# Kernel optimization log

Hardware: AMD Instinct MI355X
Metric: run time of the kernel (lower is better)

Reference implementation:

```python
import jax, jax.numpy as jnp
import numpy as np

B, M, N, E, H, HID = 4, 512, 512, 256, 16, 16
D = E // H


def setup_inputs() -> dict:
    key = jax.random.key(0)
    ks = jax.random.split(key, 10)
    u = lambda k, shape, lim: jax.random.uniform(k, shape, jnp.float32, -lim, lim)
    mix1_init = (1.0 / 2.0) ** 0.5
    mix2_init = (1.0 / 16.0) ** 0.5
    return {
        "q_input": jax.random.normal(ks[0], (B, M, E), jnp.float32),
        "kv_input": jax.random.normal(ks[1], (B, N, E), jnp.float32),
        "dmat": jax.random.uniform(ks[2], (B, M, N), jnp.float32),
        "Wq": u(ks[3], (E, E), 1.0 / np.sqrt(E)),
        "Wkv": u(ks[4], (2 * E, E), 1.0 / np.sqrt(E)),
        "mix_W1": u(ks[5], (H, 2, HID), mix1_init),
        "mix_b1": u(ks[6], (H, HID), mix1_init),
        "mix_W2": u(ks[7], (H, HID, 1), mix2_init),
        "mix_b2": u(ks[8], (H, 1), mix2_init),
        "Wout": u(ks[9], (E, E), 1.0 / np.sqrt(E)),
    }


def reference(q_input, kv_input, dmat, Wq, Wkv, mix_W1, mix_b1, mix_W2, mix_b2, Wout):
    b, m, e = q_input.shape
    n = kv_input.shape[1]
    h = mix_W1.shape[0]
    d = e // h
    # projections (torch Linear: y = x @ W.T)
    q = (q_input @ Wq.T).reshape(b, m, h, d).transpose(0, 2, 1, 3)        # b h m d
    kv = (kv_input @ Wkv.T).reshape(b, n, 2, h, d)                        # (two h d) split
    k = kv[:, :, 0].transpose(0, 2, 1, 3)                                 # b h n d
    v = kv[:, :, 1].transpose(0, 2, 1, 3)                                 # b h n d
    scale = jnp.sqrt(jnp.asarray(d, q.dtype))
    scores = jnp.einsum('bhmd,bhnd->bhmn', q, k) / scale                  # b h m n
    # mix scores with dmat via per-head 2-layer MLP on the last (size-2) axis
    mix = jnp.stack([scores, jnp.broadcast_to(dmat[:, None], scores.shape)], axis=-1)  # b h m n 2
    hidden = jax.nn.relu(jnp.einsum('bhmnt,htk->bhmnk', mix, mix_W1)
                         + mix_b1[None, :, None, None, :])                # b h m n HID
    mixed = (jnp.einsum('bhmnk,hko->bhmno', hidden, mix_W2)
             + mix_b2[None, :, None, None, :])[..., 0]                    # b h m n
    probs = jax.nn.softmax(mixed, axis=-1)
    out = jnp.einsum('bhmn,bhnd->bhmd', probs, v)                         # b h m d
    out = out.transpose(0, 2, 1, 3).reshape(b, m, e)                      # b m (h d)
    return out @ Wout.T
```

## Files before the change

kernel.cpp:

```cpp
#include <hip/hip_runtime.h>
#include <stdint.h>
#include <stddef.h>

#define MM 512
#define NN 512
#define EE 256
#define HH 16
#define DD 16

typedef __bf16 bf16x8 __attribute__((ext_vector_type(8)));
typedef float f32x4 __attribute__((ext_vector_type(4)));

static __device__ __forceinline__ bf16x8 bzero8() {
  bf16x8 z;
#pragma unroll
  for (int i = 0; i < 8; ++i) z[i] = (__bf16)0.0f;
  return z;
}

static __device__ __forceinline__ bf16x8 cvt8(const float* __restrict__ p) {
  const float4 u = *(const float4*)p;
  const float4 v = *(const float4*)(p + 4);
  bf16x8 r;
  r[0] = (__bf16)u.x; r[1] = (__bf16)u.y; r[2] = (__bf16)u.z; r[3] = (__bf16)u.w;
  r[4] = (__bf16)v.x; r[5] = (__bf16)v.y; r[6] = (__bf16)v.z; r[7] = (__bf16)v.w;
  return r;
}

static __device__ __forceinline__ unsigned short f2b(float f) {
  union { __bf16 h; unsigned short u; } cv;
  cv.h = (__bf16)f;
  return cv.u;
}

static __device__ __forceinline__ float b2f(unsigned short u) {
  union { unsigned int i; float f; } cv;
  cv.i = ((unsigned int)u) << 16;
  return cv.f;
}

static __device__ __forceinline__ float fexp2(float x) {
  float r;
  asm("v_exp_f32 %0, %1" : "=v"(r) : "v"(x));
  return r;
}

static __device__ __forceinline__ unsigned int cvtpk(float lo, float hi) {
  unsigned int r;
  asm("v_cvt_pk_bf16_f32 %0, %1, %2" : "=v"(r) : "v"(lo), "v"(hi));
  return r;
}

static __device__ __forceinline__ float sload(const float* p) {
  return __int_as_float(__builtin_amdgcn_readfirstlane(__float_as_int(*p)));
}

__global__ __launch_bounds__(256) void proj_all_kernel(
    const float* __restrict__ Xq, const float* __restrict__ Xkv,
    const float* __restrict__ Wq, const float* __restrict__ Wkv,
    const float* __restrict__ Wout,
    unsigned short* __restrict__ Qs, unsigned short* __restrict__ Ks,
    unsigned short* __restrict__ Vt,
    unsigned short* __restrict__ Whi, unsigned short* __restrict__ Wlo) {
  const int by = blockIdx.y;
  const int tid = threadIdx.x;

  if (by == 12) {
    const int base = (blockIdx.x * 256 + tid) * 4;
    const float4 v = *(const float4*)(Wout + base);
    float c4[4] = {v.x, v.y, v.z, v.w};
#pragma unroll
    for (int i = 0; i < 4; ++i) {
      const unsigned short hb = f2b(c4[i]);
      Whi[base + i] = hb;
      Wlo[base + i] = f2b(c4[i] - b2f(hb));
    }
    return;
  }

  const int w = tid >> 6, l = tid & 63;
  const int lg = l >> 4, lr = l & 15;
  const int t0 = blockIdx.x * 32 + (w & 1) * 16;

  if (by < 4) {
    const int n0 = by * 64 + (w >> 1) * 32;
    f32x4 acc0 = {0.f, 0.f, 0.f, 0.f}, acc1 = {0.f, 0.f, 0.f, 0.f};
#pragma unroll
    for (int kc = 0; kc < EE; kc += 32) {
      const int k = kc + lg * 8;
      bf16x8 a  = cvt8(Xq + (size_t)(t0 + lr) * EE + k);
      bf16x8 b0 = cvt8(Wq + (size_t)(n0 + lr) * EE + k);
      bf16x8 b1 = cvt8(Wq + (size_t)(n0 + 16 + lr) * EE + k);
      acc0 = __builtin_amdgcn_mfma_f32_16x16x32_bf16(a, b0, acc0, 0, 0, 0);
      acc1 = __builtin_amdgcn_mfma_f32_16x16x32_bf16(a, b1, acc1, 0, 0, 0);
    }
#pragma unroll
    for (int r = 0; r < 4; ++r) {
      const int t = t0 + 4 * lg + r, b = t >> 9, m = t & 511;
      const int j0 = n0 + lr, j1 = j0 + 16;
      Qs[((size_t)(b * HH + (j0 >> 4)) * MM + m) * DD + (j0 & 15)] = f2b(acc0[r] * 0.25f);
      Qs[((size_t)(b * HH + (j1 >> 4)) * MM + m) * DD + (j1 & 15)] = f2b(acc1[r] * 0.25f);
    }
  } else {
    const int n0 = (by - 4) * 64 + (w >> 1) * 32;
    f32x4 acc0 = {0.f, 0.f, 0.f, 0.f}, acc1 = {0.f, 0.f, 0.f, 0.f};
#pragma unroll
    for (int kc = 0; kc < EE; kc += 32) {
      const int k = kc + lg * 8;
      bf16x8 a  = cvt8(Xkv + (size_t)(t0 + lr) * EE + k);
      bf16x8 b0 = cvt8(Wkv + (size_t)(n0 + lr) * EE + k);
      bf16x8 b1 = cvt8(Wkv + (size_t)(n0 + 16 + lr) * EE + k);
      acc0 = __builtin_amdgcn_mfma_f32_16x16x32_bf16(a, b0, acc0, 0, 0, 0);
      acc1 = __builtin_amdgcn_mfma_f32_16x16x32_bf16(a, b1, acc1, 0, 0, 0);
    }
#pragma unroll
    for (int r = 0; r < 4; ++r) {
      const int t = t0 + 4 * lg + r, b = t >> 9, n = t & 511;
#pragma unroll
      for (int fi = 0; fi < 2; ++fi) {
        const int j = n0 + lr + fi * 16;
        const float v = fi ? acc1[r] : acc0[r];
        if (j < 256) {
          Ks[((size_t)(b * HH + (j >> 4)) * NN + n) * DD + (j & 15)] = f2b(v);
        } else {
          const int jj = j - 256;
          Vt[((size_t)(b * HH + (jj >> 4)) * DD + (jj & 15)) * NN + n] = f2b(v);
        }
      }
    }
  }
}

__global__ __launch_bounds__(256, 2) void attn_kernel(
    const unsigned short* __restrict__ Qs, const unsigned short* __restrict__ Ks,
    const unsigned short* __restrict__ Vt, const float* __restrict__ dmat,
    const float* __restrict__ W1, const float* __restrict__ b1v,
    const float* __restrict__ W2,
    unsigned short* __restrict__ Ahi, unsigned short* __restrict__ Alo) {
  __shared__ unsigned short P[32][520];
  __shared__ float red[4][32];
  float (*pvred)[2][16][16] = (float (*)[2][16][16]) & P[0][0];

  const int tid = threadIdx.x, w = tid >> 6, l = tid & 63;
  const int lg = l >> 4, lr = l & 15;
  const int bid = blockIdx.x;
  const int mt = bid & 15, hh = (bid >> 4) & 15, b = bid >> 8;
  const int m0 = mt * 32;
  const int n0 = w * 128;

  const unsigned short* Qbase = Qs + ((size_t)(b * HH + hh) * MM + m0) * DD;
  const unsigned short* Kbase = Ks + (size_t)(b * HH + hh) * NN * DD;
  const unsigned short* Vbase = Vt + (size_t)(b * HH + hh) * DD * NN;
  const float* dbase = dmat + (size_t)b * MM * NN;

  float ckv[16], bkv[16], wkp[16];
  float Ac = 0.f, Cc = 0.f;
  const float hiln2 = 0.5f * 1.4426950408889634f;
#pragma unroll
  for (int k = 0; k < 16; ++k) {
    const float ak = sload(W1 + hh * 32 + k);
    const float ck = sload(W1 + hh * 32 + 16 + k);
    const float bk = sload(b1v + hh * 16 + k);
    const float wk = hiln2 * sload(W2 + hh * 16 + k);
    Ac += wk * ak;
    Cc += wk * ck;
    const float ra = 1.0f / ak;
    ckv[k] = ck * ra;
    bkv[k] = bk * ra;
    wkp[k] = wk * fabsf(ak);
    asm volatile("" : "+v"(ckv[k]));
    asm volatile("" : "+v"(bkv[k]));
  }

  bf16x8 qb[2];
#pragma unroll
  for (int mb = 0; mb < 2; ++mb) {
    qb[mb] = bzero8();
    if (lg < 2) qb[mb] = *(const bf16x8*)(Qbase + (mb * 16 + lr) * DD + lg * 8);
  }

  const f32x4 zf = {0.f, 0.f, 0.f, 0.f};
  float psum[2] = {0.f, 0.f};

#pragma unroll
  for (int nb = 0; nb < 8; ++nb) {
    bf16x8 ka = bzero8();
    if (lg < 2)
      ka = *(const bf16x8*)(Kbase + (size_t)(n0 + nb * 16 + lr) * DD + lg * 8);
    f32x4 cc[2];
    cc[0] = __builtin_amdgcn_mfma_f32_16x16x32_bf16(ka, qb[0], zf, 0, 0, 0);
    cc[1] = __builtin_amdgcn_mfma_f32_16x16x32_bf16(ka, qb[1], zf, 0, 0, 0);
#pragma unroll
    for (int mb = 0; mb < 2; ++mb) {
      const int mrow = m0 + mb * 16 + lr;
      const int ncol = n0 + nb * 16 + 4 * lg;
      const float4 dv = *(const float4*)(dbase + (size_t)mrow * NN + ncol);
      float ev[4];
#pragma unroll
      for (int r = 0; r < 4; ++r) {
        const float s = cc[mb][r];
        const float d = (r == 0) ? dv.x : (r == 1) ? dv.y : (r == 2) ? dv.z : dv.w;
        float acc = fmaf(Ac, s, Cc * d);
#pragma unroll
        for (int k = 0; k < 16; ++k) {
          const float t = fmaf(ckv[k], d, bkv[k]);
          acc = fmaf(wkp[k], fabsf(s + t), acc);
        }
        const float e = fexp2(acc);
        psum[mb] += e;
        ev[r] = e;
      }
      uint2 u;
      u.x = cvtpk(ev[0], ev[1]);
      u.y = cvtpk(ev[2], ev[3]);
      *(uint2*)&P[mb * 16 + lr][n0 + nb * 16 + 4 * lg] = u;
    }
  }

#pragma unroll
  for (int mb = 0; mb < 2; ++mb) {
    psum[mb] += __shfl_xor(psum[mb], 16);
    psum[mb] += __shfl_xor(psum[mb], 32);
    if (lg == 0) red[w][mb * 16 + lr] = psum[mb];
  }

  f32x4 pv[2];
  pv[0] = zf; pv[1] = zf;
#pragma unroll
  for (int kb = 0; kb < 4; ++kb) {
    const bf16x8 vb = *(const bf16x8*)(Vbase + (size_t)lr * NN + (n0 + kb * 32 + lg * 8));
#pragma unroll
    for (int mb = 0; mb < 2; ++mb) {
      const bf16x8 pa = *(const bf16x8*)(&P[mb * 16 + lr][n0 + kb * 32 + lg * 8]);
      pv[mb] = __builtin_amdgcn_mfma_f32_16x16x32_bf16(pa, vb, pv[mb], 0, 0, 0);
    }
  }
  __syncthreads();
#pragma unroll
  for (int mb = 0; mb < 2; ++mb)
#pragma unroll
    for (int r = 0; r < 4; ++r) pvred[w][mb][4 * lg + r][lr] = pv[mb][r];
  __syncthreads();

  for (int i = tid; i < 512; i += 256) {
    const int mr = i >> 4, dd = i & 15;
    const float s = pvred[0][mr >> 4][mr & 15][dd] + pvred[1][mr >> 4][mr & 15][dd] +
                    pvred[2][mr >> 4][mr & 15][dd] + pvred[3][mr >> 4][mr & 15][dd];
    const float rs = red[0][mr] + red[1][mr] + red[2][mr] + red[3][mr];
    const float val = s / rs;
    const unsigned short hb = f2b(val);
    const size_t o = ((size_t)(b * MM) + m0 + mr) * EE + hh * DD + dd;
    Ahi[o] = hb;
    Alo[o] = f2b(val - b2f(hb));
  }
}

__global__ __launch_bounds__(256) void out_gemm_kernel(
    const unsigned short* __restrict__ Ahi, const unsigned short* __restrict__ Alo,
    const unsigned short* __restrict__ Whi, const unsigned short* __restrict__ Wlo,
    float* __restrict__ out) {
  const int tid = threadIdx.x, w = tid >> 6, l = tid & 63;
  const int lg = l >> 4, lr = l & 15;
  const int t0 = blockIdx.x * 32 + (w & 1) * 16;
  const int n0 = blockIdx.y * 64 + (w >> 1) * 32;
  f32x4 acc0 = {0.f, 0.f, 0.f, 0.f}, acc1 = {0.f, 0.f, 0.f, 0.f};
#pragma unroll
  for (int kc = 0; kc < EE; kc += 32) {
    const int k = kc + lg * 8;
    const bf16x8 ah = *(const bf16x8*)(Ahi + (size_t)(t0 + lr) * EE + k);
    const bf16x8 al = *(const bf16x8*)(Alo + (size_t)(t0 + lr) * EE + k);
    const bf16x8 bh0 = *(const bf16x8*)(Whi + (size_t)(n0 + lr) * EE + k);
    const bf16x8 bh1 = *(const bf16x8*)(Whi + (size_t)(n0 + 16 + lr) * EE + k);
    const bf16x8 bl0 = *(const bf16x8*)(Wlo + (size_t)(n0 + lr) * EE + k);
    const bf16x8 bl1 = *(const bf16x8*)(Wlo + (size_t)(n0 + 16 + lr) * EE + k);
    acc0 = __builtin_amdgcn_mfma_f32_16x16x32_bf16(ah, bh0, acc0, 0, 0, 0);
    acc0 = __builtin_amdgcn_mfma_f32_16x16x32_bf16(al, bh0, acc0, 0, 0, 0);
    acc0 = __builtin_amdgcn_mfma_f32_16x16x32_bf16(ah, bl0, acc0, 0, 0, 0);
    acc1 = __builtin_amdgcn_mfma_f32_16x16x32_bf16(ah, bh1, acc1, 0, 0, 0);
    acc1 = __builtin_amdgcn_mfma_f32_16x16x32_bf16(al, bh1, acc1, 0, 0, 0);
    acc1 = __builtin_amdgcn_mfma_f32_16x16x32_bf16(ah, bl1, acc1, 0, 0, 0);
  }
#pragma unroll
  for (int r = 0; r < 4; ++r) {
    const int row = t0 + 4 * lg + r;
    out[(size_t)row * EE + n0 + lr] = acc0[r];
    out[(size_t)row * EE + n0 + 16 + lr] = acc1[r];
  }
}

extern "C" void kernel_launch(void* const* d_in, const int* in_sizes, int n_in,
                              void* d_out, int out_size, void* d_ws, size_t ws_size,
                              hipStream_t stream) {
  const float* q_input  = (const float*)d_in[0];
  const float* kv_input = (const float*)d_in[1];
  const float* dmat     = (const float*)d_in[2];
  const float* Wq       = (const float*)d_in[3];
  const float* Wkv      = (const float*)d_in[4];
  const float* W1       = (const float*)d_in[5];
  const float* b1       = (const float*)d_in[6];
  const float* W2       = (const float*)d_in[7];
  const float* Wout     = (const float*)d_in[9];
  float* out = (float*)d_out;

  char* ws = (char*)d_ws;
  unsigned short* Qs  = (unsigned short*)(ws);
  unsigned short* Ks  = (unsigned short*)(ws + (1u << 20));
  unsigned short* Vt  = (unsigned short*)(ws + (2u << 20));
  unsigned short* Ahi = (unsigned short*)(ws + (3u << 20));
  unsigned short* Alo = (unsigned short*)(ws + (4u << 20));
  unsigned short* Whi = (unsigned short*)(ws + (5u << 20));
  unsigned short* Wlo = (unsigned short*)(ws + (5u << 20) + (1u << 17));

  proj_all_kernel<<<dim3(64, 13), 256, 0, stream>>>(q_input, kv_input, Wq, Wkv, Wout,
                                                    Qs, Ks, Vt, Whi, Wlo);
  attn_kernel<<<dim3(1024), 256, 0, stream>>>(Qs, Ks, Vt, dmat, W1, b1, W2,
                                              Ahi, Alo);
  out_gemm_kernel<<<dim3(64, 4), 256, 0, stream>>>(Ahi, Alo, Whi, Wlo, out);
}
```

Baseline: 63.35 us.

## Fuse Q projection and output GEMM into attention kernel with last-block counter

Computes the Q projection inside the attention kernel (stored in LDS), so each 512-thread block handles 4 heads for a 32-row tile and reuses the dmat tile loaded once into registers. The output projection is done by whichever block finishes last for each (batch, m-tile), found through an atomic counter, which removes a separate kernel launch. The KV projection kernel also zeroes the counters. In exchange the grid shrinks to 256 blocks, each block runs its heads one after another, and the final GEMM runs on only 64 blocks at the tail.

```diff
diff --git a/kernel.cpp b/kernel.cpp
--- a/kernel.cpp
+++ b/kernel.cpp
@@ -55,17 +55,17 @@
   return __int_as_float(__builtin_amdgcn_readfirstlane(__float_as_int(*p)));
 }
 
-__global__ __launch_bounds__(256) void proj_all_kernel(
-    const float* __restrict__ Xq, const float* __restrict__ Xkv,
-    const float* __restrict__ Wq, const float* __restrict__ Wkv,
+__global__ __launch_bounds__(256) void proj_kv_kernel(
+    const float* __restrict__ Xkv, const float* __restrict__ Wkv,
     const float* __restrict__ Wout,
-    unsigned short* __restrict__ Qs, unsigned short* __restrict__ Ks,
-    unsigned short* __restrict__ Vt,
-    unsigned short* __restrict__ Whi, unsigned short* __restrict__ Wlo) {
+    unsigned short* __restrict__ Ks, unsigned short* __restrict__ Vt,
+    unsigned short* __restrict__ Whi, unsigned short* __restrict__ Wlo,
+    unsigned int* __restrict__ cnt) {
   const int by = blockIdx.y;
   const int tid = threadIdx.x;
 
-  if (by == 12) {
+  if (by == 8) {
+    if (blockIdx.x == 0 && tid < 64) cnt[tid] = 0u;
     const int base = (blockIdx.x * 256 + tid) * 4;
     const float4 v = *(const float4*)(Wout + base);
     float c4[4] = {v.x, v.y, v.z, v.w};
@@ -81,210 +81,222 @@
   const int w = tid >> 6, l = tid & 63;
   const int lg = l >> 4, lr = l & 15;
   const int t0 = blockIdx.x * 32 + (w & 1) * 16;
-
-  if (by < 4) {
-    const int n0 = by * 64 + (w >> 1) * 32;
-    f32x4 acc0 = {0.f, 0.f, 0.f, 0.f}, acc1 = {0.f, 0.f, 0.f, 0.f};
-#pragma unroll
-    for (int kc = 0; kc < EE; kc += 32) {
-      const int k = kc + lg * 8;
-      bf16x8 a  = cvt8(Xq + (size_t)(t0 + lr) * EE + k);
-      bf16x8 b0 = cvt8(Wq + (size_t)(n0 + lr) * EE + k);
-      bf16x8 b1 = cvt8(Wq + (size_t)(n0 + 16 + lr) * EE + k);
-      acc0 = __builtin_amdgcn_mfma_f32_16x16x32_bf16(a, b0, acc0, 0, 0, 0);
-      acc1 = __builtin_amdgcn_mfma_f32_16x16x32_bf16(a, b1, acc1, 0, 0, 0);
-    }
-#pragma unroll
-    for (int r = 0; r < 4; ++r) {
-      const int t = t0 + 4 * lg + r, b = t >> 9, m = t & 511;
-      const int j0 = n0 + lr, j1 = j0 + 16;
-      Qs[((size_t)(b * HH + (j0 >> 4)) * MM + m) * DD + (j0 & 15)] = f2b(acc0[r] * 0.25f);
-      Qs[((size_t)(b * HH + (j1 >> 4)) * MM + m) * DD + (j1 & 15)] = f2b(acc1[r] * 0.25f);
-    }
-  } else {
-    const int n0 = (by - 4) * 64 + (w >> 1) * 32;
-    f32x4 acc0 = {0.f, 0.f, 0.f, 0.f}, acc1 = {0.f, 0.f, 0.f, 0.f};
-#pragma unroll
-    for (int kc = 0; kc < EE; kc += 32) {
-      const int k = kc + lg * 8;
-      bf16x8 a  = cvt8(Xkv + (size_t)(t0 + lr) * EE + k);
-      bf16x8 b0 = cvt8(Wkv + (size_t)(n0 + lr) * EE + k);
-      bf16x8 b1 = cvt8(Wkv + (size_t)(n0 + 16 + lr) * EE + k);
-      acc0 = __builtin_amdgcn_mfma_f32_16x16x32_bf16(a, b0, acc0, 0, 0, 0);
-      acc1 = __builtin_amdgcn_mfma_f32_16x16x32_bf16(a, b1, acc1, 0, 0, 0);
-    }
-#pragma unroll
-    for (int r = 0; r < 4; ++r) {
-      const int t = t0 + 4 * lg + r, b = t >> 9, n = t & 511;
-#pragma unroll
-      for (int fi = 0; fi < 2; ++fi) {
-        const int j = n0 + lr + fi * 16;
-        const float v = fi ? acc1[r] : acc0[r];
-        if (j < 256) {
-          Ks[((size_t)(b * HH + (j >> 4)) * NN + n) * DD + (j & 15)] = f2b(v);
-        } else {
-          const int jj = j - 256;
-          Vt[((size_t)(b * HH + (jj >> 4)) * DD + (jj & 15)) * NN + n] = f2b(v);
-        }
+  const int n0 = by * 64 + (w >> 1) * 32;
+  f32x4 acc0 = {0.f, 0.f, 0.f, 0.f}, acc1 = {0.f, 0.f, 0.f, 0.f};
+#pragma unroll
+  for (int kc = 0; kc < EE; kc += 32) {
+    const int k = kc + lg * 8;
+    bf16x8 a  = cvt8(Xkv + (size_t)(t0 + lr) * EE + k);
+    bf16x8 b0 = cvt8(Wkv + (size_t)(n0 + lr) * EE + k);
+    bf16x8 b1 = cvt8(Wkv + (size_t)(n0 + 16 + lr) * EE + k);
+    acc0 = __builtin_amdgcn_mfma_f32_16x16x32_bf16(a, b0, acc0, 0, 0, 0);
+    acc1 = __builtin_amdgcn_mfma_f32_16x16x32_bf16(a, b1, acc1, 0, 0, 0);
+  }
+#pragma unroll
+  for (int r = 0; r < 4; ++r) {
+    const int t = t0 + 4 * lg + r, b = t >> 9, n = t & 511;
+#pragma unroll
+    for (int fi = 0; fi < 2; ++fi) {
+      const int j = n0 + lr + fi * 16;
+      const float v = fi ? acc1[r] : acc0[r];
+      if (j < 256) {
+        Ks[((size_t)(b * HH + (j >> 4)) * NN + n) * DD + (j & 15)] = f2b(v);
+      } else {
+        const int jj = j - 256;
+        Vt[((size_t)(b * HH + (jj >> 4)) * DD + (jj & 15)) * NN + n] = f2b(v);
       }
     }
   }
 }
 
-__global__ __launch_bounds__(256, 2) void attn_kernel(
-    const unsigned short* __restrict__ Qs, const unsigned short* __restrict__ Ks,
-    const unsigned short* __restrict__ Vt, const float* __restrict__ dmat,
+__global__ __launch_bounds__(512, 2) void attn_fused_kernel(
+    const float* __restrict__ Xq, const float* __restrict__ Wq,
+    const float* __restrict__ dmat,
+    const unsigned short* __restrict__ Ks, const unsigned short* __restrict__ Vt,
     const float* __restrict__ W1, const float* __restrict__ b1v,
     const float* __restrict__ W2,
-    unsigned short* __restrict__ Ahi, unsigned short* __restrict__ Alo) {
+    unsigned short* __restrict__ Ahi, unsigned short* __restrict__ Alo,
+    const unsigned short* __restrict__ Whi, const unsigned short* __restrict__ Wlo,
+    float* __restrict__ out, unsigned int* __restrict__ cnt) {
+  __shared__ unsigned short Qlds[32][72];
   __shared__ unsigned short P[32][520];
-  __shared__ float red[4][32];
-  float (*pvred)[2][16][16] = (float (*)[2][16][16]) & P[0][0];
+  __shared__ float pvred[8][2][16][16];
+  __shared__ float red[8][32];
+  __shared__ int lastf;
 
   const int tid = threadIdx.x, w = tid >> 6, l = tid & 63;
   const int lg = l >> 4, lr = l & 15;
   const int bid = blockIdx.x;
-  const int mt = bid & 15, hh = (bid >> 4) & 15, b = bid >> 8;
+  const int hg = bid & 3, mt = (bid >> 2) & 15, b = bid >> 6;
   const int m0 = mt * 32;
-  const int n0 = w * 128;
-
-  const unsigned short* Qbase = Qs + ((size_t)(b * HH + hh) * MM + m0) * DD;
-  const unsigned short* Kbase = Ks + (size_t)(b * HH + hh) * NN * DD;
-  const unsigned short* Vbase = Vt + (size_t)(b * HH + hh) * DD * NN;
+  const int n0 = w * 64;
+
+  const f32x4 zf = {0.f, 0.f, 0.f, 0.f};
+
   const float* dbase = dmat + (size_t)b * MM * NN;
-
-  float ckv[16], bkv[16], wkp[16];
-  float Ac = 0.f, Cc = 0.f;
-  const float hiln2 = 0.5f * 1.4426950408889634f;
-#pragma unroll
-  for (int k = 0; k < 16; ++k) {
-    const float ak = sload(W1 + hh * 32 + k);
-    const float ck = sload(W1 + hh * 32 + 16 + k);
-    const float bk = sload(b1v + hh * 16 + k);
-    const float wk = hiln2 * sload(W2 + hh * 16 + k);
-    Ac += wk * ak;
-    Cc += wk * ck;
-    const float ra = 1.0f / ak;
-    ckv[k] = ck * ra;
-    bkv[k] = bk * ra;
-    wkp[k] = wk * fabsf(ak);
-    asm volatile("" : "+v"(ckv[k]));
-    asm volatile("" : "+v"(bkv[k]));
-  }
-
-  bf16x8 qb[2];
-#pragma unroll
-  for (int mb = 0; mb < 2; ++mb) {
-    qb[mb] = bzero8();
-    if (lg < 2) qb[mb] = *(const bf16x8*)(Qbase + (mb * 16 + lr) * DD + lg * 8);
-  }
-
-  const f32x4 zf = {0.f, 0.f, 0.f, 0.f};
-  float psum[2] = {0.f, 0.f};
-
-#pragma unroll
-  for (int nb = 0; nb < 8; ++nb) {
-    bf16x8 ka = bzero8();
-    if (lg < 2)
-      ka = *(const bf16x8*)(Kbase + (size_t)(n0 + nb * 16 + lr) * DD + lg * 8);
-    f32x4 cc[2];
-    cc[0] = __builtin_amdgcn_mfma_f32_16x16x32_bf16(ka, qb[0], zf, 0, 0, 0);
-    cc[1] = __builtin_amdgcn_mfma_f32_16x16x32_bf16(ka, qb[1], zf, 0, 0, 0);
+  float4 dv[4][2];
+#pragma unroll
+  for (int nb = 0; nb < 4; ++nb)
+#pragma unroll
+    for (int mb = 0; mb < 2; ++mb)
+      dv[nb][mb] = *(const float4*)(dbase + (size_t)(m0 + mb * 16 + lr) * NN +
+                                    n0 + nb * 16 + 4 * lg);
+
+  {
+    const int mi = w & 1, ci = w >> 1;
+    f32x4 acc = zf;
+#pragma unroll
+    for (int kc = 0; kc < EE; kc += 32) {
+      const int k = kc + lg * 8;
+      bf16x8 a  = cvt8(Xq + (size_t)(b * MM + m0 + mi * 16 + lr) * EE + k);
+      bf16x8 bb = cvt8(Wq + (size_t)(hg * 64 + ci * 16 + lr) * EE + k);
+      acc = __builtin_amdgcn_mfma_f32_16x16x32_bf16(a, bb, acc, 0, 0, 0);
+    }
+#pragma unroll
+    for (int r = 0; r < 4; ++r)
+      Qlds[mi * 16 + 4 * lg + r][ci * 16 + lr] = f2b(acc[r] * 0.25f);
+  }
+  __syncthreads();
+
+#pragma clang loop unroll(disable)
+  for (int j = 0; j < 4; ++j) {
+    const int hh = hg * 4 + j;
+
+    float ckv[16], bkv[16], wkp[16];
+    float Ac = 0.f, Cc = 0.f;
+    const float hiln2 = 0.5f * 1.4426950408889634f;
+#pragma unroll
+    for (int k = 0; k < 16; ++k) {
+      const float ak = sload(W1 + hh * 32 + k);
+      const float ck = sload(W1 + hh * 32 + 16 + k);
+      const float bk = sload(b1v + hh * 16 + k);
+      const float wk = hiln2 * sload(W2 + hh * 16 + k);
+      Ac += wk * ak;
+      Cc += wk * ck;
+      const float ra = 1.0f / ak;
+      ckv[k] = ck * ra;
+      bkv[k] = bk * ra;
+      wkp[k] = wk * fabsf(ak);
+      asm volatile("" : "+v"(ckv[k]));
+      asm volatile("" : "+v"(bkv[k]));
+    }
+
+    bf16x8 qb[2];
 #pragma unroll
     for (int mb = 0; mb < 2; ++mb) {
-      const int mrow = m0 + mb * 16 + lr;
-      const int ncol = n0 + nb * 16 + 4 * lg;
-      const float4 dv = *(const float4*)(dbase + (size_t)mrow * NN + ncol);
-      float ev[4];
-#pragma unroll
-      for (int r = 0; r < 4; ++r) {
-        const float s = cc[mb][r];
-        const float d = (r == 0) ? dv.x : (r == 1) ? dv.y : (r == 2) ? dv.z : dv.w;
-        float acc = fmaf(Ac, s, Cc * d);
-#pragma unroll
-        for (int k = 0; k < 16; ++k) {
-          const float t = fmaf(ckv[k], d, bkv[k]);
-          acc = fmaf(wkp[k], fabsf(s + t), acc);
+      qb[mb] = bzero8();
+      if (lg < 2)
+        qb[mb] = *(const bf16x8*)&Qlds[mb * 16 + lr][j * 16 + lg * 8];
+    }
+
+    const unsigned short* Kbase = Ks + (size_t)(b * HH + hh) * NN * DD;
+    const unsigned short* Vbase = Vt + (size_t)(b * HH + hh) * DD * NN;
+
+    float psum[2] = {0.f, 0.f};
+#pragma unroll
+    for (int nb = 0; nb < 4; ++nb) {
+      bf16x8 ka = bzero8();
+      if (lg < 2)
+        ka = *(const bf16x8*)(Kbase + (size_t)(n0 + nb * 16 + lr) * DD + lg * 8);
+      f32x4 cc[2];
+      cc[0] = __builtin_amdgcn_mfma_f32_16x16x32_bf16(ka, qb[0], zf, 0, 0, 0);
+      cc[1] = __builtin_amdgcn_mfma_f32_16x16x32_bf16(ka, qb[1], zf, 0, 0, 0);
+#pragma unroll
+      for (int mb = 0; mb < 2; ++mb) {
+        const float4 dvv = dv[nb][mb];
+        float ev[4];
+#pragma unroll
+        for (int r = 0; r < 4; ++r) {
+          const float s = cc[mb][r];
+          const float d = (r == 0) ? dvv.x : (r == 1) ? dvv.y : (r == 2) ? dvv.z : dvv.w;
+          float acc = fmaf(Ac, s, Cc * d);
+#pragma unroll
+          for (int k = 0; k < 16; ++k) {
+            const float t = fmaf(ckv[k], d, bkv[k]);
+            acc = fmaf(wkp[k], fabsf(s + t), acc);
+          }
+          const float e = fexp2(acc);
+          psum[mb] += e;
+          ev[r] = e;
         }
-        const float e = fexp2(acc);
-        psum[mb] += e;
-        ev[r] = e;
+        uint2 u;
+        u.x = cvtpk(ev[0], ev[1]);
+        u.y = cvtpk(ev[2], ev[3]);
+        *(uint2*)&P[mb * 16 + lr][n0 + nb * 16 + 4 * lg] = u;
       }
-      uint2 u;
-      u.x = cvtpk(ev[0], ev[1]);
-      u.y = cvtpk(ev[2], ev[3]);
-      *(uint2*)&P[mb * 16 + lr][n0 + nb * 16 + 4 * lg] = u;
-    }
-  }
-
-#pragma unroll
-  for (int mb = 0; mb < 2; ++mb) {
-    psum[mb] += __shfl_xor(psum[mb], 16);
-    psum[mb] += __shfl_xor(psum[mb], 32);
-    if (lg == 0) red[w][mb * 16 + lr] = psum[mb];
-  }
-
-  f32x4 pv[2];
-  pv[0] = zf; pv[1] = zf;
-#pragma unroll
-  for (int kb = 0; kb < 4; ++kb) {
-    const bf16x8 vb = *(const bf16x8*)(Vbase + (size_t)lr * NN + (n0 + kb * 32 + lg * 8));
+    }
+
 #pragma unroll
     for (int mb = 0; mb < 2; ++mb) {
-      const bf16x8 pa = *(const bf16x8*)(&P[mb * 16 + lr][n0 + kb * 32 + lg * 8]);
-      pv[mb] = __builtin_amdgcn_mfma_f32_16x16x32_bf16(pa, vb, pv[mb], 0, 0, 0);
-    }
+      psum[mb] += __shfl_xor(psum[mb], 16);
+      psum[mb] += __shfl_xor(psum[mb], 32);
+      if (lg == 0) red[w][mb * 16 + lr] = psum[mb];
+    }
+
+    f32x4 pv0 = zf, pv1 = zf;
+#pragma unroll
+    for (int kb = 0; kb < 2; ++kb) {
+      const bf16x8 vb = *(const bf16x8*)(Vbase + (size_t)lr * NN + n0 + kb * 32 + lg * 8);
+      const bf16x8 pa0 = *(const bf16x8*)&P[lr][n0 + kb * 32 + lg * 8];
+      const bf16x8 pa1 = *(const bf16x8*)&P[16 + lr][n0 + kb * 32 + lg * 8];
+      pv0 = __builtin_amdgcn_mfma_f32_16x16x32_bf16(pa0, vb, pv0, 0, 0, 0);
+      pv1 = __builtin_amdgcn_mfma_f32_16x16x32_bf16(pa1, vb, pv1, 0, 0, 0);
+    }
+#pragma unroll
+    for (int r = 0; r < 4; ++r) {
+      pvred[w][0][4 * lg + r][lr] = pv0[r];
+      pvred[w][1][4 * lg + r][lr] = pv1[r];
+    }
+    __syncthreads();
+
+    {
+      const int mr = tid >> 4, dd = tid & 15;
+      float s = 0.f, rs = 0.f;
+#pragma unroll
+      for (int ww = 0; ww < 8; ++ww) {
+        s += pvred[ww][mr >> 4][mr & 15][dd];
+        rs += red[ww][mr];
+      }
+      const float val = s / rs;
+      const unsigned short hb = f2b(val);
+      const size_t o = ((size_t)(b * MM) + m0 + mr) * EE + hh * DD + dd;
+      Ahi[o] = hb;
+      Alo[o] = f2b(val - b2f(hb));
+    }
+    __syncthreads();
+  }
+
+  if (tid == 0) {
+    __threadfence();
+    const unsigned int old = __hip_atomic_fetch_add(
+        &cnt[b * 16 + mt], 1u, __ATOMIC_ACQ_REL, __HIP_MEMORY_SCOPE_AGENT);
+    lastf = (old == 3u) ? 1 : 0;
   }
   __syncthreads();
-#pragma unroll
-  for (int mb = 0; mb < 2; ++mb)
-#pragma unroll
-    for (int r = 0; r < 4; ++r) pvred[w][mb][4 * lg + r][lr] = pv[mb][r];
-  __syncthreads();
-
-  for (int i = tid; i < 512; i += 256) {
-    const int mr = i >> 4, dd = i & 15;
-    const float s = pvred[0][mr >> 4][mr & 15][dd] + pvred[1][mr >> 4][mr & 15][dd] +
-                    pvred[2][mr >> 4][mr & 15][dd] + pvred[3][mr >> 4][mr & 15][dd];
-    const float rs = red[0][mr] + red[1][mr] + red[2][mr] + red[3][mr];
-    const float val = s / rs;
-    const unsigned short hb = f2b(val);
-    const size_t o = ((size_t)(b * MM) + m0 + mr) * EE + hh * DD + dd;
-    Ahi[o] = hb;
-    Alo[o] = f2b(val - b2f(hb));
-  }
-}
-
-__global__ __launch_bounds__(256) void out_gemm_kernel(
-    const unsigned short* __restrict__ Ahi, const unsigned short* __restrict__ Alo,
-    const unsigned short* __restrict__ Whi, const unsigned short* __restrict__ Wlo,
-    float* __restrict__ out) {
-  const int tid = threadIdx.x, w = tid >> 6, l = tid & 63;
-  const int lg = l >> 4, lr = l & 15;
-  const int t0 = blockIdx.x * 32 + (w & 1) * 16;
-  const int n0 = blockIdx.y * 64 + (w >> 1) * 32;
-  f32x4 acc0 = {0.f, 0.f, 0.f, 0.f}, acc1 = {0.f, 0.f, 0.f, 0.f};
-#pragma unroll
-  for (int kc = 0; kc < EE; kc += 32) {
-    const int k = kc + lg * 8;
-    const bf16x8 ah = *(const bf16x8*)(Ahi + (size_t)(t0 + lr) * EE + k);
-    const bf16x8 al = *(const bf16x8*)(Alo + (size_t)(t0 + lr) * EE + k);
-    const bf16x8 bh0 = *(const bf16x8*)(Whi + (size_t)(n0 + lr) * EE + k);
-    const bf16x8 bh1 = *(const bf16x8*)(Whi + (size_t)(n0 + 16 + lr) * EE + k);
-    const bf16x8 bl0 = *(const bf16x8*)(Wlo + (size_t)(n0 + lr) * EE + k);
-    const bf16x8 bl1 = *(const bf16x8*)(Wlo + (size_t)(n0 + 16 + lr) * EE + k);
-    acc0 = __builtin_amdgcn_mfma_f32_16x16x32_bf16(ah, bh0, acc0, 0, 0, 0);
-    acc0 = __builtin_amdgcn_mfma_f32_16x16x32_bf16(al, bh0, acc0, 0, 0, 0);
-    acc0 = __builtin_amdgcn_mfma_f32_16x16x32_bf16(ah, bl0, acc0, 0, 0, 0);
-    acc1 = __builtin_amdgcn_mfma_f32_16x16x32_bf16(ah, bh1, acc1, 0, 0, 0);
-    acc1 = __builtin_amdgcn_mfma_f32_16x16x32_bf16(al, bh1, acc1, 0, 0, 0);
-    acc1 = __builtin_amdgcn_mfma_f32_16x16x32_bf16(ah, bl1, acc1, 0, 0, 0);
-  }
-#pragma unroll
-  for (int r = 0; r < 4; ++r) {
-    const int row = t0 + 4 * lg + r;
-    out[(size_t)row * EE + n0 + lr] = acc0[r];
-    out[(size_t)row * EE + n0 + 16 + lr] = acc1[r];
+  if (lastf) {
+    __threadfence();
+    const int rbase = b * MM + m0 + (w & 1) * 16;
+    const int c0 = (w >> 1) * 64;
+    f32x4 acc[4] = {zf, zf, zf, zf};
+#pragma unroll
+    for (int kc = 0; kc < EE; kc += 32) {
+      const int k = kc + lg * 8;
+      const bf16x8 ah = *(const bf16x8*)(Ahi + (size_t)(rbase + lr) * EE + k);
+      const bf16x8 al = *(const bf16x8*)(Alo + (size_t)(rbase + lr) * EE + k);
+#pragma unroll
+      for (int t = 0; t < 4; ++t) {
+        const bf16x8 bh = *(const bf16x8*)(Whi + (size_t)(c0 + t * 16 + lr) * EE + k);
+        const bf16x8 bl = *(const bf16x8*)(Wlo + (size_t)(c0 + t * 16 + lr) * EE + k);
+        acc[t] = __builtin_amdgcn_mfma_f32_16x16x32_bf16(ah, bh, acc[t], 0, 0, 0);
+        acc[t] = __builtin_amdgcn_mfma_f32_16x16x32_bf16(al, bh, acc[t], 0, 0, 0);
+        acc[t] = __builtin_amdgcn_mfma_f32_16x16x32_bf16(ah, bl, acc[t], 0, 0, 0);
+      }
+    }
+#pragma unroll
+    for (int t = 0; t < 4; ++t)
+#pragma unroll
+      for (int r = 0; r < 4; ++r)
+        out[(size_t)(rbase + 4 * lg + r) * EE + c0 + t * 16 + lr] = acc[t][r];
   }
 }
 
@@ -303,17 +315,17 @@
   float* out = (float*)d_out;
 
   char* ws = (char*)d_ws;
-  unsigned short* Qs  = (unsigned short*)(ws);
-  unsigned short* Ks  = (unsigned short*)(ws + (1u << 20));
-  unsigned short* Vt  = (unsigned short*)(ws + (2u << 20));
-  unsigned short* Ahi = (unsigned short*)(ws + (3u << 20));
-  unsigned short* Alo = (unsigned short*)(ws + (4u << 20));
-  unsigned short* Whi = (unsigned short*)(ws + (5u << 20));
-  unsigned short* Wlo = (unsigned short*)(ws + (5u << 20) + (1u << 17));
-
-  proj_all_kernel<<<dim3(64, 13), 256, 0, stream>>>(q_input, kv_input, Wq, Wkv, Wout,
-                                                    Qs, Ks, Vt, Whi, Wlo);
-  attn_kernel<<<dim3(1024), 256, 0, stream>>>(Qs, Ks, Vt, dmat, W1, b1, W2,
-                                              Ahi, Alo);
-  out_gemm_kernel<<<dim3(64, 4), 256, 0, stream>>>(Ahi, Alo, Whi, Wlo, out);
-}
+  unsigned short* Ks  = (unsigned short*)(ws);
+  unsigned short* Vt  = (unsigned short*)(ws + (1u << 20));
+  unsigned short* Ahi = (unsigned short*)(ws + (2u << 20));
+  unsigned short* Alo = (unsigned short*)(ws + (3u << 20));
+  unsigned short* Whi = (unsigned short*)(ws + (4u << 20));
+  unsigned short* Wlo = (unsigned short*)(ws + (4u << 20) + (1u << 17));
+  unsigned int*   cnt = (unsigned int*)(ws + (4u << 20) + (2u << 17));
+
+  proj_kv_kernel<<<dim3(64, 9), 256, 0, stream>>>(kv_input, Wkv, Wout,
+                                                  Ks, Vt, Whi, Wlo, cnt);
+  attn_fused_kernel<<<dim3(256), 512, 0, stream>>>(q_input, Wq, dmat, Ks, Vt,
+                                                   W1, b1, W2, Ahi, Alo,
+                                                   Whi, Wlo, out, cnt);
+}
```

Result: slower. 110.1 us (+73.9%).
